# Optimization experiments

Hardware: AMD Instinct MI355X
Metric: run time of the kernel (lower is better)

Reference implementation:

```python
import jax, jax.numpy as jnp
import numpy as np

# Human3.6M 17-joint skeleton (parent of each joint; -1 = root)
_PARENTS = np.array([-1, 0, 1, 2, 0, 4, 5, 0, 7, 8, 9, 8, 11, 12, 8, 14, 15])
J = 17          # joints
C_OUT = 128     # out_features (per-channel adjacency count)
F_IN = 128      # in_features
B, T = 64, 243  # batch, frames
NEG = -9.0e15   # matches torch constant -9000000000000000.0


def _skeleton_indices():
    A = np.eye(J, dtype=np.float32)  # self-loops (SemGCN adjacency includes I)
    for i, p in enumerate(_PARENTS):
        if p >= 0:
            A[i, p] = 1.0
            A[p, i] = 1.0
    ii, jj = np.nonzero(A)  # row-major order, identical to torch adj>0 mask order
    return ii.astype(np.int32), jj.astype(np.int32)


def setup_inputs() -> dict:
    key = jax.random.key(0)
    kx, kw, ke = jax.random.split(key, 3)
    ii, jj = _skeleton_indices()  # nnz = 49
    x = jax.random.normal(kx, (B, T, J, F_IN), dtype=jnp.float32)
    # xavier_uniform with gain=1.414 over (2, in, out)
    bound = 1.414 * np.sqrt(6.0 / (F_IN + C_OUT))
    W = jax.random.uniform(kw, (2, F_IN, C_OUT), dtype=jnp.float32,
                           minval=-bound, maxval=bound)
    e = jax.random.uniform(ke, (C_OUT, ii.shape[0]), dtype=jnp.float32)
    return {"x": x, "W": W, "e": e,
            "idx_i": jnp.asarray(ii), "idx_j": jnp.asarray(jj)}


def reference(x, W, e, idx_i, idx_j):
    # x: [B,T,J,F_in], W: [2,F_in,C], e: [C,nnz]
    C = e.shape[0]
    nj = x.shape[2]
    h0 = jnp.einsum('btji,io->btjo', x, W[0])  # [B,T,J,C]
    h1 = jnp.einsum('btji,io->btjo', x, W[1])  # [B,T,J,C]
    # dense per-channel adjacency: masked scatter of e, then row softmax
    adj = jnp.full((C, nj, nj), NEG, dtype=x.dtype)
    adj = adj.at[:, idx_i, idx_j].set(e)
    adj = jax.nn.softmax(adj, axis=2)  # [C,J,J]
    # diagonal part: (adj*E) @ h0  ==  elementwise scale by diag entries
    d = jnp.diagonal(adj, axis1=1, axis2=2)        # [C,J]
    eye = jnp.eye(nj, dtype=x.dtype)
    off = adj * (1.0 - eye)                         # [C,J,J]
    out = h0 * d.T[None, None] + jnp.einsum('cjk,btkc->btjc', off, h1)
    return out  # [B,T,J,C]
```

## Files before the change

kernel.cpp:

```cpp
#include <hip/hip_runtime.h>

#define NJ   17
#define FD   128
#define NC   128
#define NNZ  49
#define FPT  16
#define XROW (NJ*FD)
#define WS_WT 65536

typedef __attribute__((ext_vector_type(8))) short bf16x8;
typedef __attribute__((ext_vector_type(4))) float f32x4;

__device__ __forceinline__ ushort f2bf(float f) {
  unsigned u = __float_as_uint(f);
  u = (u + 0x7fffu + ((u >> 16) & 1u)) >> 16;
  return (ushort)u;
}
__device__ __forceinline__ float bf2f(ushort s) {
  return __uint_as_float(((unsigned)s) << 16);
}
__device__ __forceinline__ unsigned cvtpk(float a, float b) {
  unsigned r;
  asm("v_cvt_pk_bf16_f32 %0, %1, %2" : "=v"(r) : "v"(a), "v"(b));
  return r;
}
__device__ __forceinline__ bf16x8 pack8(float4 a, float4 b) {
  union { unsigned u[4]; bf16x8 v; } r;
  r.u[0] = cvtpk(a.x, a.y); r.u[1] = cvtpk(a.z, a.w);
  r.u[2] = cvtpk(b.x, b.y); r.u[3] = cvtpk(b.z, b.w);
  return r.v;
}
__device__ __forceinline__ void axpy(f32x4& o, float s, f32x4 h) {
  o[0] += s * h[0]; o[1] += s * h[1]; o[2] += s * h[2]; o[3] += s * h[3];
}

struct CI { int col, dk, n, jl[3], kk[3]; };
constexpr CI TAB0[9] = {
  {0,  0, 3, {1,4,7}, {4,12,20}},
  {1,  5, 2, {0,2,0}, {1,7,0}},
  {2,  8, 2, {1,3,0}, {6,10,0}},
  {3, 11, 1, {2,0,0}, {9,0,0}},
  {4, 13, 2, {0,5,0}, {2,15,0}},
  {5, 16, 2, {4,6,0}, {14,18,0}},
  {6, 19, 1, {5,0,0}, {17,0,0}},
  {7, 21, 1, {0,0,0}, {3,0,0}},
  {8, -1, 1, {7,0,0}, {22,0,0}},
};
constexpr CI TAB1[10] = {
  {7, -1, 1, {0,0,0}, {23,0,0}},
  {8, 24, 3, {1,3,6}, {28,33,41}},
  {9, 29, 2, {0,2,0}, {25,31,0}},
  {10,32, 1, {1,0,0}, {30,0,0}},
  {11,34, 2, {0,4,0}, {26,36,0}},
  {12,37, 2, {3,5,0}, {35,39,0}},
  {13,40, 1, {4,0,0}, {38,0,0}},
  {14,42, 2, {0,7,0}, {27,44,0}},
  {15,45, 2, {6,8,0}, {43,47,0}},
  {16,48, 1, {7,0,0}, {46,0,0}},
};
constexpr int RP[NJ + 1] = {0,4,7,10,12,15,18,20,23,28,31,33,36,39,41,44,47,49};

constexpr int FL0[9][2]  = {{-1,-1},{-1,-1},{1,-1},{2,3},{-1,-1},
                            {4,-1},{5,6},{0,-1},{7,-1}};
constexpr int FL1[10][2] = {{-1,-1},{-1,-1},{-1,-1},{1,2},{-1,-1},
                            {3,-1},{4,5},{0,-1},{6,-1},{7,8}};

__global__ void prep_pack_kernel(const float* __restrict__ W,
                                 const float* __restrict__ e,
                                 bf16x8* __restrict__ Wpack,
                                 ushort* __restrict__ wt) {
  const int tid = threadIdx.x;
  if (blockIdx.x < 16) {
    const int idx = blockIdx.x * 256 + tid, n = idx >> 4, kb = idx & 15;
    const float* Wp = W + (size_t)(n >> 7) * (FD * NC) + (n & 127);
    bf16x8 v;
#pragma unroll
    for (int q = 0; q < 8; ++q) v[q] = (short)f2bf(Wp[(size_t)(kb * 8 + q) * NC]);
    Wpack[idx] = v;
  } else if (tid < NC) {
    const int c = tid;
    for (int j = 0; j < NJ; ++j) {
      const int k0 = RP[j], k1 = RP[j + 1];
      float m = -1e30f;
      for (int k = k0; k < k1; ++k) m = fmaxf(m, e[c * NNZ + k]);
      float s = 0.f;
      for (int k = k0; k < k1; ++k) s += expf(e[c * NNZ + k] - m);
      const float inv = 1.f / s;
      for (int k = k0; k < k1; ++k) wt[c * 64 + k] = f2bf(expf(e[c * NNZ + k] - m) * inv);
    }
    for (int k = NNZ; k < 64; ++k) wt[c * 64 + k] = 0;
  }
}

template <int HALF>
__device__ __forceinline__ void run(const float* __restrict__ x,
                                    const bf16x8* __restrict__ Wpack,
                                    const ushort* __restrict__ wt,
                                    float* __restrict__ out,
                                    short* xs, int tile, int cg, int tid) {
  constexpr int COL0 = HALF ? 7 : 0;
  constexpr int NCOL = HALF ? 10 : 9;
  constexpr int JN   = HALF ? 9 : 8;
  constexpr int JB   = HALF ? 8 : 0;
  constexpr int NW   = HALF ? 5 : 3;
  constexpr int WB   = HALF ? 2 : 0;
  const CI* TT = HALF ? TAB1 : TAB0;
  const int (*FL)[2] = HALF ? FL1 : FL0;

  const int w = tid >> 6, lane = tid & 63, l15 = lane & 15, l4 = lane >> 4;
  const int c = cg * 64 + w * 16 + l15;

  bf16x8 bfr[2][4];
#pragma unroll
  for (int sel = 0; sel < 2; ++sel)
#pragma unroll
    for (int ks = 0; ks < 4; ++ks)
      bfr[sel][ks] = Wpack[(sel * 128 + c) * 16 + ks * 4 + l4];
  bf16x8 wtp[NW];
#pragma unroll
  for (int r = 0; r < NW; ++r)
    wtp[r] = *(const bf16x8*)(wt + c * 64 + (WB + r) * 8);

  const float* xt = x + (size_t)tile * (FPT * XROW) + COL0 * FD;
  float4 v[12];

#define LOADP(I, S) do {                                                  \
    const int g_ = tid + (I) * 256;                                       \
    const int fr_ = g_ / (NCOL * 16), rem_ = g_ - fr_ * (NCOL * 16);      \
    const float* sp_ = xt + (size_t)fr_ * XROW + rem_ * 8;                \
    v[(S)] = *(const float4*)sp_; v[(S) + 1] = *(const float4*)(sp_ + 4); \
  } while (0)
#define STWP(I, S) do {                                                   \
    const int g_ = tid + (I) * 256;                                       \
    const int fr_ = g_ / (NCOL * 16);                                     \
    const int byte_ = (g_ * 16) ^ ((fr_ & 7) << 4);                       \
    *(bf16x8*)((char*)xs + byte_) = pack8(v[(S)], v[(S) + 1]);            \
  } while (0)

  LOADP(0, 0); LOADP(1, 2); LOADP(2, 4);
  LOADP(3, 6); LOADP(4, 8); LOADP(5, 10);
  STWP(0, 0); STWP(1, 2); STWP(2, 4);
  LOADP(6, 0); LOADP(7, 2); LOADP(8, 4);
  STWP(3, 6); STWP(4, 8); STWP(5, 10);
  if (HALF) LOADP(9, 6);
  STWP(6, 0); STWP(7, 2); STWP(8, 4);
  if (HALF) STWP(9, 6);
  __syncthreads();

  f32x4 oa[JN];
#pragma unroll
  for (int j = 0; j < JN; ++j) oa[j] = (f32x4){0.f, 0.f, 0.f, 0.f};

  float* const ob = out + (size_t)tile * (FPT * XROW);

#pragma unroll
  for (int ci = 0; ci < NCOL; ++ci) {
    const int dk = TT[ci].dk, nn = TT[ci].n;
    bf16x8 af[4];
#pragma unroll
    for (int ks = 0; ks < 4; ++ks) {
      const int byte = l15 * (NCOL * 256) + ci * 256 +
                       (((ks * 4 + l4) * 16) ^ ((l15 & 7) << 4));
      af[ks] = *(const bf16x8*)((const char*)xs + byte);
    }
    f32x4 h1 = (f32x4){0.f, 0.f, 0.f, 0.f};
#pragma unroll
    for (int ks = 0; ks < 4; ++ks)
      h1 = __builtin_amdgcn_mfma_f32_16x16x32_bf16(af[ks], bfr[1][ks], h1, 0, 0, 0);
    if (dk >= 0) {
      f32x4 h0 = (f32x4){0.f, 0.f, 0.f, 0.f};
#pragma unroll
      for (int ks = 0; ks < 4; ++ks)
        h0 = __builtin_amdgcn_mfma_f32_16x16x32_bf16(af[ks], bfr[0][ks], h0, 0, 0, 0);
      axpy(oa[TT[ci].col - JB], bf2f((ushort)wtp[(dk >> 3) - WB][dk & 7]), h0);
    }
#pragma unroll
    for (int o = 0; o < 3; ++o)
      if (o < nn)
        axpy(oa[TT[ci].jl[o]],
             bf2f((ushort)wtp[(TT[ci].kk[o] >> 3) - WB][TT[ci].kk[o] & 7]), h1);

#pragma unroll
    for (int fi = 0; fi < 2; ++fi) {
      const int fj = FL[ci][fi];
      if (fj >= 0) {
#pragma unroll
        for (int q = 0; q < 4; ++q)
          ob[(size_t)(l4 * 4 + q) * XROW + (JB + fj) * FD + c] = oa[fj][q];
      }
    }
  }
#undef LOADP
#undef STWP
}

__global__ __launch_bounds__(256, 4) void fused_kernel(
    const float*  __restrict__ x,
    const bf16x8* __restrict__ Wpack,
    const ushort* __restrict__ wt,
    float*        __restrict__ out) {
  __shared__ __align__(16) short xs[FPT * 10 * FD];
  const int tile = blockIdx.x >> 2;
  const int half = (blockIdx.x >> 1) & 1;
  const int cg   = blockIdx.x & 1;
  if (half) run<1>(x, Wpack, wt, out, xs, tile, cg, threadIdx.x);
  else      run<0>(x, Wpack, wt, out, xs, tile, cg, threadIdx.x);
}

extern "C" void kernel_launch(void* const* d_in, const int* in_sizes, int n_in,
                              void* d_out, int out_size, void* d_ws, size_t ws_size,
                              hipStream_t stream) {
  const float* x = (const float*)d_in[0];
  const float* W = (const float*)d_in[1];
  const float* e = (const float*)d_in[2];
  float* out = (float*)d_out;

  bf16x8* Wpack = (bf16x8*)d_ws;
  ushort* wt    = (ushort*)((char*)d_ws + WS_WT);

  prep_pack_kernel<<<17, 256, 0, stream>>>(W, e, Wpack, wt);

  const int frames = in_sizes[0] / XROW;
  const int ntiles = frames / FPT;
  fused_kernel<<<ntiles * 4, 256, 0, stream>>>(x, Wpack, wt, out);
}
```

Baseline: 107.4 us.

## Make blocks persistent over four tiles with double-buffered LDS prefetch

Each block now has 512 threads covering all 128 output channels, so the x tile is loaded and converted once per half instead of twice. It also loops over four consecutive frame tiles, double-buffering the bf16 x tile in LDS and issuing the next tile's global loads and LDS stores while MFMA work on the current tile runs. The goal is to halve redundant x reads and hide global load latency behind compute. In exchange the grid has 8x fewer blocks, each block needs 80 KB of LDS, and the tile count must divide evenly by four or the trailing tiles are silently dropped.

```diff
diff --git a/kernel.cpp b/kernel.cpp
--- a/kernel.cpp
+++ b/kernel.cpp
@@ -6,6 +6,8 @@
 #define NNZ  49
 #define FPT  16
 #define XROW (NJ*FD)
+#define TPB  4
+#define BUFB 40960
 #define WS_WT 65536
 
 typedef __attribute__((ext_vector_type(8))) short bf16x8;
@@ -33,6 +35,10 @@
 __device__ __forceinline__ void axpy(f32x4& o, float s, f32x4 h) {
   o[0] += s * h[0]; o[1] += s * h[1]; o[2] += s * h[2]; o[3] += s * h[3];
 }
+
+#define BARR() do { asm volatile("s_waitcnt lgkmcnt(0)" ::: "memory"); \
+                    __builtin_amdgcn_s_barrier(); \
+                    __builtin_amdgcn_sched_barrier(0); } while (0)
 
 struct CI { int col, dk, n, jl[3], kk[3]; };
 constexpr CI TAB0[9] = {
@@ -97,18 +103,19 @@
                                     const bf16x8* __restrict__ Wpack,
                                     const ushort* __restrict__ wt,
                                     float* __restrict__ out,
-                                    short* xs, int tile, int cg, int tid) {
+                                    char* b0, char* b1, int group, int tid) {
   constexpr int COL0 = HALF ? 7 : 0;
   constexpr int NCOL = HALF ? 10 : 9;
   constexpr int JN   = HALF ? 9 : 8;
   constexpr int JB   = HALF ? 8 : 0;
   constexpr int NW   = HALF ? 5 : 3;
   constexpr int WB   = HALF ? 2 : 0;
+  constexpr int NGRP = FPT * NCOL * 16;
   const CI* TT = HALF ? TAB1 : TAB0;
   const int (*FL)[2] = HALF ? FL1 : FL0;
 
   const int w = tid >> 6, lane = tid & 63, l15 = lane & 15, l4 = lane >> 4;
-  const int c = cg * 64 + w * 16 + l15;
+  const int c = w * 16 + l15;
 
   bf16x8 bfr[2][4];
 #pragma unroll
@@ -121,90 +128,108 @@
   for (int r = 0; r < NW; ++r)
     wtp[r] = *(const bf16x8*)(wt + c * 64 + (WB + r) * 8);
 
-  const float* xt = x + (size_t)tile * (FPT * XROW) + COL0 * FD;
-  float4 v[12];
-
-#define LOADP(I, S) do {                                                  \
-    const int g_ = tid + (I) * 256;                                       \
+  float4 v[2][2];
+
+#define LOADC(T, K) do {                                                  \
+    int g_ = tid + (K) * 512;                                             \
+    if ((K) >= 4 && g_ > NGRP - 1) g_ = NGRP - 1;                         \
     const int fr_ = g_ / (NCOL * 16), rem_ = g_ - fr_ * (NCOL * 16);      \
-    const float* sp_ = xt + (size_t)fr_ * XROW + rem_ * 8;                \
-    v[(S)] = *(const float4*)sp_; v[(S) + 1] = *(const float4*)(sp_ + 4); \
+    const float* sp_ = x + ((size_t)(T) * FPT + fr_) * XROW +             \
+                       COL0 * FD + rem_ * 8;                              \
+    v[(K) & 1][0] = *(const float4*)sp_;                                  \
+    v[(K) & 1][1] = *(const float4*)(sp_ + 4);                            \
   } while (0)
-#define STWP(I, S) do {                                                   \
-    const int g_ = tid + (I) * 256;                                       \
-    const int fr_ = g_ / (NCOL * 16);                                     \
-    const int byte_ = (g_ * 16) ^ ((fr_ & 7) << 4);                       \
-    *(bf16x8*)((char*)xs + byte_) = pack8(v[(S)], v[(S) + 1]);            \
+
+#define STWC(K, BUF) do {                                                 \
+    const int g_ = tid + (K) * 512;                                       \
+    if ((K) < 4 || g_ < NGRP) {                                           \
+      const int fr_ = g_ / (NCOL * 16);                                   \
+      const int byte_ = (g_ * 16) ^ ((fr_ & 7) << 4);                     \
+      *(bf16x8*)((BUF) + byte_) = pack8(v[(K) & 1][0], v[(K) & 1][1]);    \
+    }                                                                     \
   } while (0)
 
-  LOADP(0, 0); LOADP(1, 2); LOADP(2, 4);
-  LOADP(3, 6); LOADP(4, 8); LOADP(5, 10);
-  STWP(0, 0); STWP(1, 2); STWP(2, 4);
-  LOADP(6, 0); LOADP(7, 2); LOADP(8, 4);
-  STWP(3, 6); STWP(4, 8); STWP(5, 10);
-  if (HALF) LOADP(9, 6);
-  STWP(6, 0); STWP(7, 2); STWP(8, 4);
-  if (HALF) STWP(9, 6);
-  __syncthreads();
+  const int t0 = group * TPB;
+
+  LOADC(t0, 0); LOADC(t0, 1);
+  STWC(0, b0); LOADC(t0, 2);
+  STWC(1, b0); LOADC(t0, 3);
+  STWC(2, b0); LOADC(t0, 4);
+  STWC(3, b0); STWC(4, b0);
+  BARR();
 
   f32x4 oa[JN];
 #pragma unroll
   for (int j = 0; j < JN; ++j) oa[j] = (f32x4){0.f, 0.f, 0.f, 0.f};
 
-  float* const ob = out + (size_t)tile * (FPT * XROW);
-
-#pragma unroll
-  for (int ci = 0; ci < NCOL; ++ci) {
-    const int dk = TT[ci].dk, nn = TT[ci].n;
-    bf16x8 af[4];
-#pragma unroll
-    for (int ks = 0; ks < 4; ++ks) {
-      const int byte = l15 * (NCOL * 256) + ci * 256 +
-                       (((ks * 4 + l4) * 16) ^ ((l15 & 7) << 4));
-      af[ks] = *(const bf16x8*)((const char*)xs + byte);
+#pragma unroll
+  for (int i = 0; i < TPB; ++i) {
+    const char* cur = (i & 1) ? b1 : b0;
+    char* nxt = (i & 1) ? b0 : b1;
+    const int t = t0 + i;
+    const bool more = (i + 1 < TPB);
+    float* const ob = out + (size_t)t * (FPT * XROW);
+
+#pragma unroll
+    for (int ci = 0; ci < NCOL; ++ci) {
+      if (more) {
+        if (ci >= 2 && ci - 2 < 5) STWC(ci - 2, nxt);
+        if (ci < 5) LOADC(t + 1, ci);
+      }
+      const int dk = TT[ci].dk, nn = TT[ci].n;
+      bf16x8 af[4];
+#pragma unroll
+      for (int ks = 0; ks < 4; ++ks) {
+        const int byte = l15 * (NCOL * 256) + ci * 256 +
+                         (((ks * 4 + l4) * 16) ^ ((l15 & 7) << 4));
+        af[ks] = *(const bf16x8*)(cur + byte);
+      }
+      f32x4 h1 = (f32x4){0.f, 0.f, 0.f, 0.f};
+#pragma unroll
+      for (int ks = 0; ks < 4; ++ks)
+        h1 = __builtin_amdgcn_mfma_f32_16x16x32_bf16(af[ks], bfr[1][ks], h1, 0, 0, 0);
+      if (dk >= 0) {
+        f32x4 h0 = (f32x4){0.f, 0.f, 0.f, 0.f};
+#pragma unroll
+        for (int ks = 0; ks < 4; ++ks)
+          h0 = __builtin_amdgcn_mfma_f32_16x16x32_bf16(af[ks], bfr[0][ks], h0, 0, 0, 0);
+        axpy(oa[TT[ci].col - JB], bf2f((ushort)wtp[(dk >> 3) - WB][dk & 7]), h0);
+      }
+#pragma unroll
+      for (int o = 0; o < 3; ++o)
+        if (o < nn)
+          axpy(oa[TT[ci].jl[o]],
+               bf2f((ushort)wtp[(TT[ci].kk[o] >> 3) - WB][TT[ci].kk[o] & 7]), h1);
+
+#pragma unroll
+      for (int fi = 0; fi < 2; ++fi) {
+        const int fj = FL[ci][fi];
+        if (fj >= 0) {
+#pragma unroll
+          for (int q = 0; q < 4; ++q)
+            ob[(size_t)(l4 * 4 + q) * XROW + (JB + fj) * FD + c] = oa[fj][q];
+          oa[fj] = (f32x4){0.f, 0.f, 0.f, 0.f};
+        }
+      }
+      __builtin_amdgcn_sched_barrier(0);
     }
-    f32x4 h1 = (f32x4){0.f, 0.f, 0.f, 0.f};
-#pragma unroll
-    for (int ks = 0; ks < 4; ++ks)
-      h1 = __builtin_amdgcn_mfma_f32_16x16x32_bf16(af[ks], bfr[1][ks], h1, 0, 0, 0);
-    if (dk >= 0) {
-      f32x4 h0 = (f32x4){0.f, 0.f, 0.f, 0.f};
-#pragma unroll
-      for (int ks = 0; ks < 4; ++ks)
-        h0 = __builtin_amdgcn_mfma_f32_16x16x32_bf16(af[ks], bfr[0][ks], h0, 0, 0, 0);
-      axpy(oa[TT[ci].col - JB], bf2f((ushort)wtp[(dk >> 3) - WB][dk & 7]), h0);
-    }
-#pragma unroll
-    for (int o = 0; o < 3; ++o)
-      if (o < nn)
-        axpy(oa[TT[ci].jl[o]],
-             bf2f((ushort)wtp[(TT[ci].kk[o] >> 3) - WB][TT[ci].kk[o] & 7]), h1);
-
-#pragma unroll
-    for (int fi = 0; fi < 2; ++fi) {
-      const int fj = FL[ci][fi];
-      if (fj >= 0) {
-#pragma unroll
-        for (int q = 0; q < 4; ++q)
-          ob[(size_t)(l4 * 4 + q) * XROW + (JB + fj) * FD + c] = oa[fj][q];
-      }
-    }
+    BARR();
   }
-#undef LOADP
-#undef STWP
-}
-
-__global__ __launch_bounds__(256, 4) void fused_kernel(
+#undef LOADC
+#undef STWC
+}
+
+__global__ __launch_bounds__(512, 4) void fused_kernel(
     const float*  __restrict__ x,
     const bf16x8* __restrict__ Wpack,
     const ushort* __restrict__ wt,
     float*        __restrict__ out) {
-  __shared__ __align__(16) short xs[FPT * 10 * FD];
-  const int tile = blockIdx.x >> 2;
-  const int half = (blockIdx.x >> 1) & 1;
-  const int cg   = blockIdx.x & 1;
-  if (half) run<1>(x, Wpack, wt, out, xs, tile, cg, threadIdx.x);
-  else      run<0>(x, Wpack, wt, out, xs, tile, cg, threadIdx.x);
+  __shared__ __align__(16) char xs[2 * BUFB];
+  const int group = blockIdx.x >> 1;
+  if (blockIdx.x & 1)
+    run<1>(x, Wpack, wt, out, xs, xs + BUFB, group, threadIdx.x);
+  else
+    run<0>(x, Wpack, wt, out, xs, xs + BUFB, group, threadIdx.x);
 }
 
 extern "C" void kernel_launch(void* const* d_in, const int* in_sizes, int n_in,
@@ -222,5 +247,6 @@
 
   const int frames = in_sizes[0] / XROW;
   const int ntiles = frames / FPT;
-  fused_kernel<<<ntiles * 4, 256, 0, stream>>>(x, Wpack, wt, out);
-}
+  const int blocks = (ntiles / TPB) * 2;
+  fused_kernel<<<blocks, 512, 0, stream>>>(x, Wpack, wt, out);
+}
```

Result: slower. 114.2 us (+6.3%).
